# Performance work log

Measured on AMD Instinct MI355X. Metric: run time of the kernel, lower is better.

Reference implementation:

```python
import jax, jax.numpy as jnp
import numpy as np


def setup_inputs() -> dict:
    key = jax.random.key(0)
    k_x, k_w1, k_w2, k_w3 = jax.random.split(key, 4)
    input_dim, hidden_dim, num_classes = 4096, 4096, 1000
    batch = 8192
    x = jax.random.normal(k_x, (batch, input_dim), dtype=jnp.float32)
    # BinaryLinear params: weight ~ N(0,1)*0.1, bias zeros
    w1 = jax.random.normal(k_w1, (hidden_dim, input_dim), dtype=jnp.float32) * 0.1
    b1 = jnp.zeros((hidden_dim,), dtype=jnp.float32)
    w2 = jax.random.normal(k_w2, (hidden_dim, hidden_dim), dtype=jnp.float32) * 0.1
    b2 = jnp.zeros((hidden_dim,), dtype=jnp.float32)
    # fc3: plain nn.Linear (kaiming-uniform-ish; any init works for a numerics baseline)
    bound = 1.0 / np.sqrt(hidden_dim)
    w3 = jax.random.uniform(k_w3, (num_classes, hidden_dim), dtype=jnp.float32, minval=-bound, maxval=bound)
    b3 = jnp.zeros((num_classes,), dtype=jnp.float32)
    return {"x": x, "w1": w1, "b1": b1, "w2": w2, "b2": b2, "w3": w3, "b3": b3}


def _binary_linear(x, w, b):
    # sign-binarize both activations and weights, then fp32 GEMM + bias
    return jnp.sign(x) @ jnp.sign(w).T + b


def reference(x, w1, b1, w2, b2, w3, b3):
    h1 = _binary_linear(x, w1, b1)          # [B, H]
    a1 = jnp.sign(h1)
    h2 = _binary_linear(a1, w2, b2)         # [B, H]
    a2 = jnp.sign(h2)
    out = a2 @ w3.T + b3                    # [B, C] plain fp32 linear
    return out
```

## Files before the change

### kernel.cpp

```cpp
#include <hip/hip_runtime.h>
#include <hip/hip_bf16.h>


typedef __attribute__((ext_vector_type(4))) float f32x4;
typedef __attribute__((ext_vector_type(4))) int   i32x4;
typedef __attribute__((ext_vector_type(8))) int   i32x8;

#define BM 128
#define BN 128

__device__ __forceinline__ void async_copy16(const void* g, void* l) {
  __builtin_amdgcn_global_load_lds(
      (const __attribute__((address_space(1))) void*)g,
      (__attribute__((address_space(3))) void*)l,
      16, 0, 0);
}

__device__ __forceinline__ char sign8(float v) {
  return (v > 0.f) ? (char)1 : ((v < 0.f) ? (char)-1 : (char)0);
}
__device__ __forceinline__ unsigned nib4(float v) {
  return (v > 0.f) ? 0x2u : ((v < 0.f) ? 0xAu : 0x0u);
}

__global__ void sign_pack_fp4(const float* __restrict__ in, unsigned* __restrict__ out, int n8) {
  int i = blockIdx.x * blockDim.x + threadIdx.x;
  if (i >= n8) return;
  const float4* p = (const float4*)in + (size_t)i * 2;
  float4 v0 = p[0], v1 = p[1];
  unsigned b0 = nib4(v0.x) | (nib4(v0.y) << 4);
  unsigned b1 = nib4(v0.z) | (nib4(v0.w) << 4);
  unsigned b2 = nib4(v1.x) | (nib4(v1.y) << 4);
  unsigned b3 = nib4(v1.z) | (nib4(v1.w) << 4);
  out[i] = b0 | (b1 << 8) | (b2 << 16) | (b3 << 24);
}

__global__ void repack_i8_fp4(const char* __restrict__ in, unsigned* __restrict__ out, int n8) {
  int i = blockIdx.x * blockDim.x + threadIdx.x;
  if (i >= n8) return;
  int2 w = ((const int2*)in)[i];
  union { int2 d; char c[8]; } u; u.d = w;
  unsigned r = 0;
#pragma unroll
  for (int j = 0; j < 8; ++j) {
    char v = u.c[j];
    unsigned nb = (v == 1) ? 0x2u : ((v == (char)-1) ? 0xAu : 0x0u);
    r |= nb << (4 * j);
  }
  out[i] = r;
}

__global__ __launch_bounds__(256)
void w3_quant(const float* __restrict__ in, char* __restrict__ out,
              float* __restrict__ scale, int rows_valid) {
  const int row = blockIdx.x;
  const int tid = threadIdx.x;
  int* orow = (int*)(out + (size_t)row * 4096);
  if (row >= rows_valid) {
#pragma unroll
    for (int j = 0; j < 4; ++j) orow[j * 256 + tid] = 0;
    if (tid == 0) scale[row] = 0.f;
    return;
  }
  const float4* p = (const float4*)(in + (size_t)row * 4096);
  float4 v[4];
  float amax = 0.f;
#pragma unroll
  for (int j = 0; j < 4; ++j) {
    v[j] = p[j * 256 + tid];
    amax = fmaxf(amax, fmaxf(fmaxf(fabsf(v[j].x), fabsf(v[j].y)),
                             fmaxf(fabsf(v[j].z), fabsf(v[j].w))));
  }
#pragma unroll
  for (int m = 32; m >= 1; m >>= 1)
    amax = fmaxf(amax, __shfl_xor(amax, m, 64));
  __shared__ float wmax[4];
  if ((tid & 63) == 0) wmax[tid >> 6] = amax;
  __syncthreads();
  const float rowmax = fmaxf(fmaxf(wmax[0], wmax[1]), fmaxf(wmax[2], wmax[3]));
  const float inv = (rowmax > 0.f) ? 127.f / rowmax : 0.f;
#pragma unroll
  for (int j = 0; j < 4; ++j) {
    int q0 = (int)rintf(v[j].x * inv);
    int q1 = (int)rintf(v[j].y * inv);
    int q2 = (int)rintf(v[j].z * inv);
    int q3 = (int)rintf(v[j].w * inv);
    unsigned r = ((unsigned)(unsigned char)(char)q0)
               | ((unsigned)(unsigned char)(char)q1 << 8)
               | ((unsigned)(unsigned char)(char)q2 << 16)
               | ((unsigned)(unsigned char)(char)q3 << 24);
    orow[j * 256 + tid] = (int)r;
  }
  if (tid == 0) scale[row] = rowmax * (1.f / 127.f);
}

__global__ __launch_bounds__(256)
void gemm_fp4(const unsigned char* __restrict__ A,
              const unsigned char* __restrict__ B,
              const float* __restrict__ bias,
              char* __restrict__ Ci8,
              int Kb, int ldc)
{
  __shared__ unsigned char As[128 * 64];
  __shared__ unsigned char Bs[128 * 64];

  const int tid  = threadIdx.x;
  const int lane = tid & 63;
  const int wid  = tid >> 6;
  const int wy   = wid >> 1;
  const int wx   = wid & 1;

  const int m0 = blockIdx.y * BM;
  const int n0 = blockIdx.x * BN;

  const int r1 = tid >> 2;
  const int r2 = r1 + 64;
  const int c1 = (tid & 3) ^ ((r1 >> 1) & 3);
  const int c2 = (tid & 3) ^ ((r2 >> 1) & 3);
  const unsigned char* Ag1 = A + (size_t)(m0 + r1) * Kb + c1 * 16;
  const unsigned char* Ag2 = A + (size_t)(m0 + r2) * Kb + c2 * 16;
  const unsigned char* Bg1 = B + (size_t)(n0 + r1) * Kb + c1 * 16;
  const unsigned char* Bg2 = B + (size_t)(n0 + r2) * Kb + c2 * 16;
  unsigned char* Asl1 = As + tid * 16;
  unsigned char* Asl2 = As + (tid + 256) * 16;
  unsigned char* Bsl1 = Bs + tid * 16;
  unsigned char* Bsl2 = Bs + (tid + 256) * 16;

  f32x4 acc[4][4];
#pragma unroll
  for (int i = 0; i < 4; ++i)
#pragma unroll
    for (int j = 0; j < 4; ++j)
      acc[i][j] = (f32x4){0.f, 0.f, 0.f, 0.f};

  const int fr  = lane & 15;
  const int kc  = lane >> 4;
  const int swz = (kc ^ ((fr >> 1) & 3)) * 16;

  for (int k0 = 0; k0 < Kb; k0 += 64) {
    async_copy16(Ag1 + k0, Asl1);
    async_copy16(Ag2 + k0, Asl2);
    async_copy16(Bg1 + k0, Bsl1);
    async_copy16(Bg2 + k0, Bsl2);
    __syncthreads();

    i32x8 a[4], b[4];
#pragma unroll
    for (int i = 0; i < 4; ++i) {
      i32x4 t = *(const i32x4*)(As + (wy * 64 + i * 16 + fr) * 64 + swz);
      a[i] = (i32x8){t[0], t[1], t[2], t[3], 0, 0, 0, 0};
    }
#pragma unroll
    for (int j = 0; j < 4; ++j) {
      i32x4 t = *(const i32x4*)(Bs + (wx * 64 + j * 16 + fr) * 64 + swz);
      b[j] = (i32x8){t[0], t[1], t[2], t[3], 0, 0, 0, 0};
    }

#pragma unroll
    for (int i = 0; i < 4; ++i)
#pragma unroll
      for (int j = 0; j < 4; ++j)
        acc[i][j] = __builtin_amdgcn_mfma_scale_f32_16x16x128_f8f6f4(
            a[i], b[j], acc[i][j],
            4, 4,
            0, 0x7f7f7f7f,
            0, 0x7f7f7f7f);
    __syncthreads();
  }

  const int ccol = lane & 15;
  const int crow = (lane >> 4) * 4;
#pragma unroll
  for (int i = 0; i < 4; ++i) {
    const int m = m0 + wy * 64 + i * 16 + crow;
#pragma unroll
    for (int j = 0; j < 4; ++j) {
      const int n = n0 + wx * 64 + j * 16 + ccol;
      const float bv = bias[n];
#pragma unroll
      for (int r = 0; r < 4; ++r) {
        float v = acc[i][j][r] + bv;
        Ci8[(size_t)(m + r) * ldc + n] = sign8(v);
      }
    }
  }
}

__global__ __launch_bounds__(256)
void gemm_i8(const char* __restrict__ A,
             const char* __restrict__ B,
             const float* __restrict__ scale,
             const float* __restrict__ bias,
             float* __restrict__ Cf,
             int Kb, int ldc, int nvalid)
{
  __shared__ char As[128 * 64];
  __shared__ char Bs[128 * 64];

  const int tid  = threadIdx.x;
  const int lane = tid & 63;
  const int wid  = tid >> 6;
  const int wy   = wid >> 1;
  const int wx   = wid & 1;

  const int m0 = blockIdx.y * BM;
  const int n0 = blockIdx.x * BN;

  const int r1 = tid >> 2;
  const int r2 = r1 + 64;
  const int c1 = (tid & 3) ^ ((r1 >> 1) & 3);
  const int c2 = (tid & 3) ^ ((r2 >> 1) & 3);
  const char* Ag1 = A + (size_t)(m0 + r1) * Kb + c1 * 16;
  const char* Ag2 = A + (size_t)(m0 + r2) * Kb + c2 * 16;
  const char* Bg1 = B + (size_t)(n0 + r1) * Kb + c1 * 16;
  const char* Bg2 = B + (size_t)(n0 + r2) * Kb + c2 * 16;
  char* Asl1 = As + tid * 16;
  char* Asl2 = As + (tid + 256) * 16;
  char* Bsl1 = Bs + tid * 16;
  char* Bsl2 = Bs + (tid + 256) * 16;

  i32x4 acc[4][4];
#pragma unroll
  for (int i = 0; i < 4; ++i)
#pragma unroll
    for (int j = 0; j < 4; ++j)
      acc[i][j] = (i32x4){0, 0, 0, 0};

  const int fr  = lane & 15;
  const int kc  = lane >> 4;
  const int swz = (kc ^ ((fr >> 1) & 3)) * 16;

  for (int k0 = 0; k0 < Kb; k0 += 64) {
    async_copy16(Ag1 + k0, Asl1);
    async_copy16(Ag2 + k0, Asl2);
    async_copy16(Bg1 + k0, Bsl1);
    async_copy16(Bg2 + k0, Bsl2);
    __syncthreads();

    i32x4 a[4], b[4];
#pragma unroll
    for (int i = 0; i < 4; ++i)
      a[i] = *(const i32x4*)(As + (wy * 64 + i * 16 + fr) * 64 + swz);
#pragma unroll
    for (int j = 0; j < 4; ++j)
      b[j] = *(const i32x4*)(Bs + (wx * 64 + j * 16 + fr) * 64 + swz);

#pragma unroll
    for (int i = 0; i < 4; ++i)
#pragma unroll
      for (int j = 0; j < 4; ++j)
        acc[i][j] = __builtin_amdgcn_mfma_i32_16x16x64_i8(a[i], b[j], acc[i][j], 0, 0, 0);
    __syncthreads();
  }

  const int ccol = lane & 15;
  const int crow = (lane >> 4) * 4;
#pragma unroll
  for (int i = 0; i < 4; ++i) {
    const int m = m0 + wy * 64 + i * 16 + crow;
#pragma unroll
    for (int j = 0; j < 4; ++j) {
      const int n = n0 + wx * 64 + j * 16 + ccol;
      if (n >= nvalid) continue;
      const float sv = scale[n];
      const float bv = bias[n];
#pragma unroll
      for (int r = 0; r < 4; ++r) {
        Cf[(size_t)(m + r) * ldc + n] = (float)acc[i][j][r] * sv + bv;
      }
    }
  }
}

extern "C" void kernel_launch(void* const* d_in, const int* in_sizes, int n_in,
                              void* d_out, int out_size, void* d_ws, size_t ws_size,
                              hipStream_t stream) {
  const float* x  = (const float*)d_in[0];
  const float* w1 = (const float*)d_in[1];
  const float* b1 = (const float*)d_in[2];
  const float* w2 = (const float*)d_in[3];
  const float* b2 = (const float*)d_in[4];
  const float* w3 = (const float*)d_in[5];
  const float* b3 = (const float*)d_in[6];

  const int Mb = 8192, H = 4096, C = 1000, Cpad = 1024;
  const int Kb = H / 2;

  char* ws = (char*)d_ws;
  unsigned*       xp  = (unsigned*)(ws);
  unsigned*       w1p = (unsigned*)(ws + (size_t)16777216);
  unsigned*       w2p = (unsigned*)(ws + (size_t)25165824);
  char*           w3q = ws + (size_t)33554432;
  float*          s3  = (float*)(ws + (size_t)37748736);
  char*           a1  = ws + (size_t)41943040;
  unsigned*       a1p = (unsigned*)(ws + (size_t)75497472);
  char*           a2  = ws + (size_t)92274688;

  sign_pack_fp4<<<(Mb * H / 8 + 255) / 256, 256, 0, stream>>>(x,  xp,  Mb * H / 8);
  sign_pack_fp4<<<(H * H / 8 + 255) / 256, 256, 0, stream>>>(w1, w1p, H * H / 8);
  sign_pack_fp4<<<(H * H / 8 + 255) / 256, 256, 0, stream>>>(w2, w2p, H * H / 8);
  w3_quant<<<Cpad, 256, 0, stream>>>(w3, w3q, s3, C);

  dim3 blk(256);
  gemm_fp4<<<dim3(H / BN, Mb / BM), blk, 0, stream>>>(
      (const unsigned char*)xp, (const unsigned char*)w1p, b1, a1, Kb, H);
  repack_i8_fp4<<<(Mb * H / 8 + 255) / 256, 256, 0, stream>>>(a1, a1p, Mb * H / 8);
  gemm_fp4<<<dim3(H / BN, Mb / BM), blk, 0, stream>>>(
      (const unsigned char*)a1p, (const unsigned char*)w2p, b2, a2, Kb, H);
  gemm_i8<<<dim3(Cpad / BN, Mb / BM), blk, 0, stream>>>(
      a2, w3q, s3, b3, (float*)d_out, H, C, C);
}
```

Baseline: 551.3 us.

## Double-buffer GEMM LDS tiles, swizzle block order, fuse FP4 repack into epilogue

Both GEMM kernels now use two LDS buffers, so the async global-to-LDS copy for the next K tile is issued before computing the current one. Each loop iteration keeps one barrier instead of two. Block indices are remapped in groups of eight to improve L2 reuse. The first FP4 GEMM now packs its sign outputs straight into FP4 nibbles using lane shuffles, which removes the separate int8 write, the repack kernel and its memory round-trip. The cost is twice the LDS per block, which may lower occupancy, plus extra shuffle work in the epilogue.

```diff
diff --git a/kernel.cpp b/kernel.cpp
--- a/kernel.cpp
+++ b/kernel.cpp
@@ -35,21 +35,6 @@
   out[i] = b0 | (b1 << 8) | (b2 << 16) | (b3 << 24);
 }
 
-__global__ void repack_i8_fp4(const char* __restrict__ in, unsigned* __restrict__ out, int n8) {
-  int i = blockIdx.x * blockDim.x + threadIdx.x;
-  if (i >= n8) return;
-  int2 w = ((const int2*)in)[i];
-  union { int2 d; char c[8]; } u; u.d = w;
-  unsigned r = 0;
-#pragma unroll
-  for (int j = 0; j < 8; ++j) {
-    char v = u.c[j];
-    unsigned nb = (v == 1) ? 0x2u : ((v == (char)-1) ? 0xAu : 0x0u);
-    r |= nb << (4 * j);
-  }
-  out[i] = r;
-}
-
 __global__ __launch_bounds__(256)
 void w3_quant(const float* __restrict__ in, char* __restrict__ out,
               float* __restrict__ scale, int rows_valid) {
@@ -94,15 +79,64 @@
   if (tid == 0) scale[row] = rowmax * (1.f / 127.f);
 }
 
+
+__device__ __forceinline__ void fp4_compute(const unsigned char* Asb,
+                                            const unsigned char* Bsb,
+                                            int wy, int wx, int fr, int swz,
+                                            f32x4 (&acc)[4][4]) {
+  i32x8 a[4], b[4];
+#pragma unroll
+  for (int i = 0; i < 4; ++i) {
+    i32x4 t = *(const i32x4*)(Asb + (wy * 64 + i * 16 + fr) * 64 + swz);
+    a[i] = (i32x8){t[0], t[1], t[2], t[3], 0, 0, 0, 0};
+  }
+#pragma unroll
+  for (int j = 0; j < 4; ++j) {
+    i32x4 t = *(const i32x4*)(Bsb + (wx * 64 + j * 16 + fr) * 64 + swz);
+    b[j] = (i32x8){t[0], t[1], t[2], t[3], 0, 0, 0, 0};
+  }
+#pragma unroll
+  for (int i = 0; i < 4; ++i)
+#pragma unroll
+    for (int j = 0; j < 4; ++j)
+      acc[i][j] = __builtin_amdgcn_mfma_scale_f32_16x16x128_f8f6f4(
+          a[i], b[j], acc[i][j],
+          4, 4,
+          0, 0x7f7f7f7f,
+          0, 0x7f7f7f7f);
+}
+
+__device__ __forceinline__ void i8_compute(const char* Asb, const char* Bsb,
+                                           int wy, int wx, int fr, int swz,
+                                           i32x4 (&acc)[4][4]) {
+  i32x4 a[4], b[4];
+#pragma unroll
+  for (int i = 0; i < 4; ++i)
+    a[i] = *(const i32x4*)(Asb + (wy * 64 + i * 16 + fr) * 64 + swz);
+#pragma unroll
+  for (int j = 0; j < 4; ++j)
+    b[j] = *(const i32x4*)(Bsb + (wx * 64 + j * 16 + fr) * 64 + swz);
+#pragma unroll
+  for (int i = 0; i < 4; ++i)
+#pragma unroll
+    for (int j = 0; j < 4; ++j)
+      acc[i][j] = __builtin_amdgcn_mfma_i32_16x16x64_i8(a[i], b[j], acc[i][j], 0, 0, 0);
+}
+
+template <int EPI>
 __global__ __launch_bounds__(256)
 void gemm_fp4(const unsigned char* __restrict__ A,
               const unsigned char* __restrict__ B,
               const float* __restrict__ bias,
+              unsigned* __restrict__ Cp4,
               char* __restrict__ Ci8,
-              int Kb, int ldc)
+              int ldc)
 {
-  __shared__ unsigned char As[128 * 64];
-  __shared__ unsigned char Bs[128 * 64];
+  constexpr int KB  = 2048;
+  constexpr int NIT = KB / 64;
+
+  __shared__ unsigned char As[2][128 * 64];
+  __shared__ unsigned char Bs[2][128 * 64];
 
   const int tid  = threadIdx.x;
   const int lane = tid & 63;
@@ -110,21 +144,20 @@
   const int wy   = wid >> 1;
   const int wx   = wid & 1;
 
-  const int m0 = blockIdx.y * BM;
-  const int n0 = blockIdx.x * BN;
+  const int nwg  = gridDim.x * gridDim.y;
+  const int flat = blockIdx.y * gridDim.x + blockIdx.x;
+  const int swzb = (flat & 7) * (nwg >> 3) + (flat >> 3);
+  const int m0   = (swzb / gridDim.x) * BM;
+  const int n0   = (swzb % gridDim.x) * BN;
 
   const int r1 = tid >> 2;
   const int r2 = r1 + 64;
   const int c1 = (tid & 3) ^ ((r1 >> 1) & 3);
   const int c2 = (tid & 3) ^ ((r2 >> 1) & 3);
-  const unsigned char* Ag1 = A + (size_t)(m0 + r1) * Kb + c1 * 16;
-  const unsigned char* Ag2 = A + (size_t)(m0 + r2) * Kb + c2 * 16;
-  const unsigned char* Bg1 = B + (size_t)(n0 + r1) * Kb + c1 * 16;
-  const unsigned char* Bg2 = B + (size_t)(n0 + r2) * Kb + c2 * 16;
-  unsigned char* Asl1 = As + tid * 16;
-  unsigned char* Asl2 = As + (tid + 256) * 16;
-  unsigned char* Bsl1 = Bs + tid * 16;
-  unsigned char* Bsl2 = Bs + (tid + 256) * 16;
+  const unsigned char* Ag1 = A + (size_t)(m0 + r1) * KB + c1 * 16;
+  const unsigned char* Ag2 = A + (size_t)(m0 + r2) * KB + c2 * 16;
+  const unsigned char* Bg1 = B + (size_t)(n0 + r1) * KB + c1 * 16;
+  const unsigned char* Bg2 = B + (size_t)(n0 + r2) * KB + c2 * 16;
 
   f32x4 acc[4][4];
 #pragma unroll
@@ -137,50 +170,64 @@
   const int kc  = lane >> 4;
   const int swz = (kc ^ ((fr >> 1) & 3)) * 16;
 
-  for (int k0 = 0; k0 < Kb; k0 += 64) {
-    async_copy16(Ag1 + k0, Asl1);
-    async_copy16(Ag2 + k0, Asl2);
-    async_copy16(Bg1 + k0, Bsl1);
-    async_copy16(Bg2 + k0, Bsl2);
+#define STAGE_FP4(buf, k0)                                   \
+  do {                                                       \
+    async_copy16(Ag1 + (k0), &As[buf][tid * 16]);            \
+    async_copy16(Ag2 + (k0), &As[buf][(tid + 256) * 16]);    \
+    async_copy16(Bg1 + (k0), &Bs[buf][tid * 16]);            \
+    async_copy16(Bg2 + (k0), &Bs[buf][(tid + 256) * 16]);    \
+  } while (0)
+
+  STAGE_FP4(0, 0);
+  __syncthreads();
+
+#pragma unroll
+  for (int it = 0; it < NIT - 1; ++it) {
+    const int cur = it & 1;
+    STAGE_FP4(cur ^ 1, (it + 1) * 64);
+    fp4_compute(As[cur], Bs[cur], wy, wx, fr, swz, acc);
     __syncthreads();
-
-    i32x8 a[4], b[4];
-#pragma unroll
-    for (int i = 0; i < 4; ++i) {
-      i32x4 t = *(const i32x4*)(As + (wy * 64 + i * 16 + fr) * 64 + swz);
-      a[i] = (i32x8){t[0], t[1], t[2], t[3], 0, 0, 0, 0};
-    }
-#pragma unroll
-    for (int j = 0; j < 4; ++j) {
-      i32x4 t = *(const i32x4*)(Bs + (wx * 64 + j * 16 + fr) * 64 + swz);
-      b[j] = (i32x8){t[0], t[1], t[2], t[3], 0, 0, 0, 0};
-    }
-
-#pragma unroll
-    for (int i = 0; i < 4; ++i)
-#pragma unroll
-      for (int j = 0; j < 4; ++j)
-        acc[i][j] = __builtin_amdgcn_mfma_scale_f32_16x16x128_f8f6f4(
-            a[i], b[j], acc[i][j],
-            4, 4,
-            0, 0x7f7f7f7f,
-            0, 0x7f7f7f7f);
-    __syncthreads();
-  }
+  }
+  fp4_compute(As[(NIT - 1) & 1], Bs[(NIT - 1) & 1], wy, wx, fr, swz, acc);
+#undef STAGE_FP4
 
   const int ccol = lane & 15;
   const int crow = (lane >> 4) * 4;
-#pragma unroll
-  for (int i = 0; i < 4; ++i) {
-    const int m = m0 + wy * 64 + i * 16 + crow;
-#pragma unroll
-    for (int j = 0; j < 4; ++j) {
-      const int n = n0 + wx * 64 + j * 16 + ccol;
-      const float bv = bias[n];
+
+  if (EPI == 1) {
+#pragma unroll
+    for (int i = 0; i < 4; ++i) {
+      const int m = m0 + wy * 64 + i * 16 + crow;
+#pragma unroll
+      for (int j = 0; j < 4; ++j) {
+        const int n = n0 + wx * 64 + j * 16 + ccol;
+        const float bv = bias[n];
+#pragma unroll
+        for (int r = 0; r < 4; ++r)
+          Ci8[(size_t)(m + r) * ldc + n] = sign8(acc[i][j][r] + bv);
+      }
+    }
+  } else {
+#pragma unroll
+    for (int i = 0; i < 4; ++i) {
+      const int m = m0 + wy * 64 + i * 16 + crow;
 #pragma unroll
       for (int r = 0; r < 4; ++r) {
-        float v = acc[i][j][r] + bv;
-        Ci8[(size_t)(m + r) * ldc + n] = sign8(v);
+        unsigned w32[4];
+#pragma unroll
+        for (int j = 0; j < 4; ++j) {
+          const int n = n0 + wx * 64 + j * 16 + ccol;
+          unsigned nb = nib4(acc[i][j][r] + bias[n]);
+          unsigned pb = nb | (((unsigned)__shfl_xor((int)nb, 1)) << 4);
+          unsigned w  = pb | (((unsigned)__shfl_xor((int)pb, 2)) << 8);
+          w32[j]      = w  | (((unsigned)__shfl_xor((int)w,  4)) << 16);
+        }
+        if ((ccol & 7) == 0) {
+          const size_t rowb = (size_t)(m + r) * (ldc >> 3);
+#pragma unroll
+          for (int j = 0; j < 4; ++j)
+            Cp4[rowb + ((n0 + wx * 64 + j * 16 + ccol) >> 3)] = w32[j];
+        }
       }
     }
   }
@@ -192,10 +239,13 @@
              const float* __restrict__ scale,
              const float* __restrict__ bias,
              float* __restrict__ Cf,
-             int Kb, int ldc, int nvalid)
+             int ldc, int nvalid)
 {
-  __shared__ char As[128 * 64];
-  __shared__ char Bs[128 * 64];
+  constexpr int KB  = 4096;
+  constexpr int NIT = KB / 64;
+
+  __shared__ char As[2][128 * 64];
+  __shared__ char Bs[2][128 * 64];
 
   const int tid  = threadIdx.x;
   const int lane = tid & 63;
@@ -203,21 +253,20 @@
   const int wy   = wid >> 1;
   const int wx   = wid & 1;
 
-  const int m0 = blockIdx.y * BM;
-  const int n0 = blockIdx.x * BN;
+  const int nwg  = gridDim.x * gridDim.y;
+  const int flat = blockIdx.y * gridDim.x + blockIdx.x;
+  const int swzb = (flat & 7) * (nwg >> 3) + (flat >> 3);
+  const int m0   = (swzb / gridDim.x) * BM;
+  const int n0   = (swzb % gridDim.x) * BN;
 
   const int r1 = tid >> 2;
   const int r2 = r1 + 64;
   const int c1 = (tid & 3) ^ ((r1 >> 1) & 3);
   const int c2 = (tid & 3) ^ ((r2 >> 1) & 3);
-  const char* Ag1 = A + (size_t)(m0 + r1) * Kb + c1 * 16;
-  const char* Ag2 = A + (size_t)(m0 + r2) * Kb + c2 * 16;
-  const char* Bg1 = B + (size_t)(n0 + r1) * Kb + c1 * 16;
-  const char* Bg2 = B + (size_t)(n0 + r2) * Kb + c2 * 16;
-  char* Asl1 = As + tid * 16;
-  char* Asl2 = As + (tid + 256) * 16;
-  char* Bsl1 = Bs + tid * 16;
-  char* Bsl2 = Bs + (tid + 256) * 16;
+  const char* Ag1 = A + (size_t)(m0 + r1) * KB + c1 * 16;
+  const char* Ag2 = A + (size_t)(m0 + r2) * KB + c2 * 16;
+  const char* Bg1 = B + (size_t)(n0 + r1) * KB + c1 * 16;
+  const char* Bg2 = B + (size_t)(n0 + r2) * KB + c2 * 16;
 
   i32x4 acc[4][4];
 #pragma unroll
@@ -230,28 +279,26 @@
   const int kc  = lane >> 4;
   const int swz = (kc ^ ((fr >> 1) & 3)) * 16;
 
-  for (int k0 = 0; k0 < Kb; k0 += 64) {
-    async_copy16(Ag1 + k0, Asl1);
-    async_copy16(Ag2 + k0, Asl2);
-    async_copy16(Bg1 + k0, Bsl1);
-    async_copy16(Bg2 + k0, Bsl2);
+#define STAGE_I8(buf, k0)                                    \
+  do {                                                       \
+    async_copy16(Ag1 + (k0), &As[buf][tid * 16]);            \
+    async_copy16(Ag2 + (k0), &As[buf][(tid + 256) * 16]);    \
+    async_copy16(Bg1 + (k0), &Bs[buf][tid * 16]);            \
+    async_copy16(Bg2 + (k0), &Bs[buf][(tid + 256) * 16]);    \
+  } while (0)
+
+  STAGE_I8(0, 0);
+  __syncthreads();
+
+#pragma unroll 8
+  for (int it = 0; it < NIT - 1; ++it) {
+    const int cur = it & 1;
+    STAGE_I8(cur ^ 1, (it + 1) * 64);
+    i8_compute(As[cur], Bs[cur], wy, wx, fr, swz, acc);
     __syncthreads();
-
-    i32x4 a[4], b[4];
-#pragma unroll
-    for (int i = 0; i < 4; ++i)
-      a[i] = *(const i32x4*)(As + (wy * 64 + i * 16 + fr) * 64 + swz);
-#pragma unroll
-    for (int j = 0; j < 4; ++j)
-      b[j] = *(const i32x4*)(Bs + (wx * 64 + j * 16 + fr) * 64 + swz);
-
-#pragma unroll
-    for (int i = 0; i < 4; ++i)
-#pragma unroll
-      for (int j = 0; j < 4; ++j)
-        acc[i][j] = __builtin_amdgcn_mfma_i32_16x16x64_i8(a[i], b[j], acc[i][j], 0, 0, 0);
-    __syncthreads();
-  }
+  }
+  i8_compute(As[(NIT - 1) & 1], Bs[(NIT - 1) & 1], wy, wx, fr, swz, acc);
+#undef STAGE_I8
 
   const int ccol = lane & 15;
   const int crow = (lane >> 4) * 4;
@@ -265,9 +312,8 @@
       const float sv = scale[n];
       const float bv = bias[n];
 #pragma unroll
-      for (int r = 0; r < 4; ++r) {
+      for (int r = 0; r < 4; ++r)
         Cf[(size_t)(m + r) * ldc + n] = (float)acc[i][j][r] * sv + bv;
-      }
     }
   }
 }
@@ -284,17 +330,15 @@
   const float* b3 = (const float*)d_in[6];
 
   const int Mb = 8192, H = 4096, C = 1000, Cpad = 1024;
-  const int Kb = H / 2;
 
   char* ws = (char*)d_ws;
-  unsigned*       xp  = (unsigned*)(ws);
-  unsigned*       w1p = (unsigned*)(ws + (size_t)16777216);
-  unsigned*       w2p = (unsigned*)(ws + (size_t)25165824);
-  char*           w3q = ws + (size_t)33554432;
-  float*          s3  = (float*)(ws + (size_t)37748736);
-  char*           a1  = ws + (size_t)41943040;
-  unsigned*       a1p = (unsigned*)(ws + (size_t)75497472);
-  char*           a2  = ws + (size_t)92274688;
+  unsigned* xp  = (unsigned*)(ws);
+  unsigned* w1p = (unsigned*)(ws + (size_t)16777216);
+  unsigned* w2p = (unsigned*)(ws + (size_t)25165824);
+  char*     w3q = ws + (size_t)33554432;
+  float*    s3  = (float*)(ws + (size_t)37748736);
+  unsigned* a1p = (unsigned*)(ws + (size_t)41943040);
+  char*     a2  = ws + (size_t)58720256;
 
   sign_pack_fp4<<<(Mb * H / 8 + 255) / 256, 256, 0, stream>>>(x,  xp,  Mb * H / 8);
   sign_pack_fp4<<<(H * H / 8 + 255) / 256, 256, 0, stream>>>(w1, w1p, H * H / 8);
@@ -302,11 +346,10 @@
   w3_quant<<<Cpad, 256, 0, stream>>>(w3, w3q, s3, C);
 
   dim3 blk(256);
-  gemm_fp4<<<dim3(H / BN, Mb / BM), blk, 0, stream>>>(
-      (const unsigned char*)xp, (const unsigned char*)w1p, b1, a1, Kb, H);
-  repack_i8_fp4<<<(Mb * H / 8 + 255) / 256, 256, 0, stream>>>(a1, a1p, Mb * H / 8);
-  gemm_fp4<<<dim3(H / BN, Mb / BM), blk, 0, stream>>>(
-      (const unsigned char*)a1p, (const unsigned char*)w2p, b2, a2, Kb, H);
+  gemm_fp4<0><<<dim3(H / BN, Mb / BM), blk, 0, stream>>>(
+      (const unsigned char*)xp, (const unsigned char*)w1p, b1, a1p, nullptr, H);
+  gemm_fp4<1><<<dim3(H / BN, Mb / BM), blk, 0, stream>>>(
+      (const unsigned char*)a1p, (const unsigned char*)w2p, b2, nullptr, a2, H);
   gemm_i8<<<dim3(Cpad / BN, Mb / BM), blk, 0, stream>>>(
-      a2, w3q, s3, b3, (float*)d_out, H, C, C);
-}
+      a2, w3q, s3, b3, (float*)d_out, C, C);
+}
```

New measurement: 652.4 us. +18.3%, slower.
